# Kernel tuning notes

Measured on AMD Instinct MI355X. Metric: run time of the kernel, lower is better.

The kernel has to match this reference:

```python
import jax, jax.numpy as jnp
import numpy as np

N_NODES = 100000
N_EDGES = 6400000


def setup_inputs() -> dict:
    key = jax.random.key(0)
    ks = jax.random.split(key, 8)
    x = jax.random.normal(ks[0], (N_NODES, 1), dtype=jnp.float32)
    edge_index = jax.random.randint(ks[1], (2, N_EDGES), 0, N_NODES, dtype=jnp.int64)
    # lin1: Linear(1, 16); lin2: Linear(16, 1); sage lin_l: Linear(1, 2, bias=False)
    W1 = jax.random.normal(ks[2], (16, 1), dtype=jnp.float32) * 0.5
    b1 = jax.random.normal(ks[3], (16,), dtype=jnp.float32) * 0.1
    W2 = jax.random.normal(ks[4], (1, 16), dtype=jnp.float32) * 0.25
    b2 = jax.random.normal(ks[5], (1,), dtype=jnp.float32) * 0.1
    Ws = jax.random.normal(ks[6], (2, 1), dtype=jnp.float32) * 0.5
    return {"x": x, "W1": W1, "b1": b1, "W2": W2, "b2": b2, "Ws": Ws,
            "edge_index": edge_index}


def reference(x, W1, b1, W2, b2, Ws, edge_index):
    # tiny MLP: Linear(1,16) -> ReLU -> Linear(16,1)
    h = jax.nn.relu(x @ W1.T + b1) @ W2.T + b2              # [N, 1]
    src, dst = edge_index[0], edge_index[1]
    # SAGEConv mean aggregation: mean of source features per target node
    msg = h[src]                                            # [E, 1] gather
    agg = jax.ops.segment_sum(msg, dst, num_segments=N_NODES)   # [N, 1]
    cnt = jax.ops.segment_sum(jnp.ones((src.shape[0],), jnp.float32), dst,
                              num_segments=N_NODES)         # [N]
    mean = agg / jnp.maximum(cnt, 1.0)[:, None]             # zero for isolated nodes
    # lin_l (root_weight=False, bias=False)
    return mean @ Ws.T                                      # [N, 2]
```

## Files before the change

kernel.cpp:

```cpp
#include <hip/hip_runtime.h>

#define N_NODES 100000
#define N_EDGES 6400000

#define HSCALE 4096.0f
#define HCLAMP 63.0f
#define HBIAS  (1 << 19)

#define QBIN       4096
#define QBIN_SHIFT 12
#define NQBINS     25
#define PBLOCKS    512
#define PTHREADS   1024
#define LCAP       640
#define GBINCAP    270336
#define NQBLK      20
#define QTHREADS   1024

__global__ void mlp_kernel(const float* __restrict__ x,
                           const float* __restrict__ W1,
                           const float* __restrict__ b1,
                           const float* __restrict__ W2,
                           const float* __restrict__ b2,
                           int* __restrict__ hfix, int n) {
    int i = blockIdx.x * blockDim.x + threadIdx.x;
    if (i >= n) return;
    float xv = x[i];
    float acc = b2[0];
#pragma unroll
    for (int k = 0; k < 16; ++k) {
        float t = fmaxf(W1[k] * xv + b1[k], 0.0f);
        acc = fmaf(W2[k], t, acc);
    }
    acc = fminf(fmaxf(acc, -HCLAMP), HCLAMP);
    hfix[i] = __float2int_rn(acc * HSCALE);
}

__global__ __launch_bounds__(PTHREADS)
void partition_kernel(const int* __restrict__ src,
                      const int* __restrict__ dst,
                      const int* __restrict__ hfix,
                      unsigned* __restrict__ recs,
                      unsigned* __restrict__ cursor) {
    extern __shared__ unsigned sbuf[];
    __shared__ unsigned scnt[NQBINS];
    __shared__ unsigned sbase[NQBINS];
    const int tid = threadIdx.x;
    if (tid < NQBINS) scnt[tid] = 0u;
    __syncthreads();

    const int quads = (N_EDGES / 4) / PBLOCKS;
    const int4* __restrict__ s4 = (const int4*)src + (size_t)blockIdx.x * quads;
    const int4* __restrict__ d4 = (const int4*)dst + (size_t)blockIdx.x * quads;

    for (int i = tid; i < quads; i += PTHREADS) {
        int4 d = d4[i];
        int4 s = s4[i];
        unsigned v0 = (unsigned)(hfix[s.x] + HBIAS);
        unsigned v1 = (unsigned)(hfix[s.y] + HBIAS);
        unsigned v2 = (unsigned)(hfix[s.z] + HBIAS);
        unsigned v3 = (unsigned)(hfix[s.w] + HBIAS);
        int b0 = d.x >> QBIN_SHIFT, b1 = d.y >> QBIN_SHIFT;
        int b2 = d.z >> QBIN_SHIFT, b3 = d.w >> QBIN_SHIFT;
        unsigned rec0 = ((unsigned)(d.x & (QBIN - 1)) << 20) | v0;
        unsigned rec1 = ((unsigned)(d.y & (QBIN - 1)) << 20) | v1;
        unsigned rec2 = ((unsigned)(d.z & (QBIN - 1)) << 20) | v2;
        unsigned rec3 = ((unsigned)(d.w & (QBIN - 1)) << 20) | v3;
        unsigned sl0 = atomicAdd(&scnt[b0], 1u);
        unsigned sl1 = atomicAdd(&scnt[b1], 1u);
        unsigned sl2 = atomicAdd(&scnt[b2], 1u);
        unsigned sl3 = atomicAdd(&scnt[b3], 1u);
#define STORE(B, SL, REC)                                                     \
        if ((SL) < (unsigned)LCAP) {                                          \
            sbuf[(B) * LCAP + (SL)] = (REC);                                  \
        } else {                                                              \
            unsigned g = atomicAdd(&cursor[B], 1u);                           \
            if (g < (unsigned)GBINCAP) recs[(size_t)(B) * GBINCAP + g] = (REC);\
        }
        STORE(b0, sl0, rec0);
        STORE(b1, sl1, rec1);
        STORE(b2, sl2, rec2);
        STORE(b3, sl3, rec3);
#undef STORE
    }
    __syncthreads();

    if (tid < NQBINS) {
        unsigned m = min(scnt[tid], (unsigned)LCAP);
        sbase[tid] = atomicAdd(&cursor[tid], m);
    }
    __syncthreads();
    for (int b = 0; b < NQBINS; ++b) {
        unsigned m = min(scnt[b], (unsigned)LCAP);
        unsigned bs = sbase[b];
        for (unsigned t = tid; t < m; t += PTHREADS) {
            unsigned g = bs + t;
            if (g < (unsigned)GBINCAP)
                recs[(size_t)b * GBINCAP + g] = sbuf[b * LCAP + t];
        }
    }
}

__global__ __launch_bounds__(QTHREADS)
void accumulate_kernel(const unsigned* __restrict__ recs,
                       const unsigned* __restrict__ cursor,
                       unsigned* __restrict__ partials) {
    __shared__ unsigned acc[QBIN];
    const int b = blockIdx.x / NQBLK;
    const int j = blockIdx.x % NQBLK;
    const int tid = threadIdx.x;
    for (int k = tid; k < QBIN; k += QTHREADS) acc[k] = 0u;
    __syncthreads();

    const unsigned total = min(cursor[b], (unsigned)GBINCAP);
    const unsigned* __restrict__ base = recs + (size_t)b * GBINCAP;
    for (unsigned i = (unsigned)j * QTHREADS + tid; i < total;
         i += (unsigned)NQBLK * QTHREADS) {
        unsigned rec = base[i];
        unsigned rel = rec >> 20;
        int hf = (int)(rec & 0xFFFFFu) - HBIAS;
        atomicAdd(&acc[rel], (((unsigned)hf) << 8) + 1u);
    }
    __syncthreads();

    unsigned* __restrict__ outp = partials + (size_t)blockIdx.x * QBIN;
    for (int k = tid; k < QBIN; k += QTHREADS) outp[k] = acc[k];
}

__global__ void finalize_part(const unsigned* __restrict__ partials,
                              const float* __restrict__ Ws,
                              float* __restrict__ out, int n) {
    int i = blockIdx.x * blockDim.x + threadIdx.x;
    if (i >= n) return;
    const int bin = i >> QBIN_SHIFT;
    const int local = i & (QBIN - 1);
    int cnt = 0, sum = 0;
#pragma unroll
    for (int j = 0; j < NQBLK; ++j) {
        unsigned p = partials[(size_t)(bin * NQBLK + j) * QBIN + local];
        cnt += (int)(p & 0xFFu);
        sum += ((int)p) >> 8;
    }
    float mean = ((float)sum * (1.0f / HSCALE)) / (float)max(cnt, 1);
    float2 o;
    o.x = mean * Ws[0];
    o.y = mean * Ws[1];
    ((float2*)out)[i] = o;
}

template <int TBIN, int TNBINS>
__global__ __launch_bounds__(1024)
void scatter_binned(const int* __restrict__ src,
                    const int* __restrict__ dst,
                    const int* __restrict__ hfix,
                    unsigned* __restrict__ partials,
                    int n4_per_slice) {
    extern __shared__ unsigned acc[];
    const int bin   = blockIdx.x % TNBINS;
    const int slice = blockIdx.x / TNBINS;
    const int tid = threadIdx.x;
    for (int j = tid; j < TBIN; j += 1024) acc[j] = 0u;
    __syncthreads();
    const int bin_lo = bin * TBIN;
    const int4* __restrict__ s4 = (const int4*)src + (size_t)slice * n4_per_slice;
    const int4* __restrict__ d4 = (const int4*)dst + (size_t)slice * n4_per_slice;
#define PROC(dd, ss)                                                          \
    {                                                                         \
        unsigned r;                                                           \
        r = (unsigned)((dd).x - bin_lo);                                      \
        if (r < (unsigned)TBIN)                                               \
            atomicAdd(&acc[r], (((unsigned)hfix[(ss).x]) << 8) + 1u);         \
        r = (unsigned)((dd).y - bin_lo);                                      \
        if (r < (unsigned)TBIN)                                               \
            atomicAdd(&acc[r], (((unsigned)hfix[(ss).y]) << 8) + 1u);         \
        r = (unsigned)((dd).z - bin_lo);                                      \
        if (r < (unsigned)TBIN)                                               \
            atomicAdd(&acc[r], (((unsigned)hfix[(ss).z]) << 8) + 1u);         \
        r = (unsigned)((dd).w - bin_lo);                                      \
        if (r < (unsigned)TBIN)                                               \
            atomicAdd(&acc[r], (((unsigned)hfix[(ss).w]) << 8) + 1u);         \
    }
    for (int i = tid; i < n4_per_slice; i += 2048) {
        int4 d0 = d4[i];
        int4 s0 = s4[i];
        const int i1 = i + 1024;
        int4 d1, s1;
        const bool have1 = i1 < n4_per_slice;
        if (have1) { d1 = d4[i1]; s1 = s4[i1]; }
        PROC(d0, s0);
        if (have1) PROC(d1, s1);
    }
#undef PROC
    __syncthreads();
    unsigned* __restrict__ outp = partials + (size_t)blockIdx.x * TBIN;
    for (int j = tid; j < TBIN; j += 1024) outp[j] = acc[j];
}

template <int TBIN, int TNBINS>
__global__ void finalize_binned(const unsigned* __restrict__ partials,
                                const float* __restrict__ Ws,
                                float* __restrict__ out, int n, int nslices) {
    int i = blockIdx.x * blockDim.x + threadIdx.x;
    if (i >= n) return;
    const int bin = i / TBIN;
    const int local = i % TBIN;
    int cnt = 0, sum = 0;
    for (int s = 0; s < nslices; ++s) {
        unsigned p = partials[(size_t)(s * TNBINS + bin) * TBIN + local];
        cnt += (int)(p & 0xFFu);
        sum += ((int)p) >> 8;
    }
    float mean = ((float)sum * (1.0f / HSCALE)) / (float)max(cnt, 1);
    float2 o;
    o.x = mean * Ws[0];
    o.y = mean * Ws[1];
    ((float2*)out)[i] = o;
}

__global__ void scatter_atomic(const int* __restrict__ src,
                               const int* __restrict__ dst,
                               const int* __restrict__ hfix,
                               unsigned long long* __restrict__ packed) {
    int tid = blockIdx.x * blockDim.x + threadIdx.x;
    int stride = gridDim.x * blockDim.x;
    const int4* __restrict__ src4 = (const int4*)src;
    const int4* __restrict__ dst4 = (const int4*)dst;
    const int n4 = N_EDGES / 4;
    for (int e = tid; e < n4; e += stride) {
        int4 s = src4[e];
        int4 d = dst4[e];
        long long h0 = hfix[s.x], h1 = hfix[s.y], h2 = hfix[s.z], h3 = hfix[s.w];
        atomicAdd(&packed[d.x], ((unsigned long long)(h0 << 20)) + 1ull);
        atomicAdd(&packed[d.y], ((unsigned long long)(h1 << 20)) + 1ull);
        atomicAdd(&packed[d.z], ((unsigned long long)(h2 << 20)) + 1ull);
        atomicAdd(&packed[d.w], ((unsigned long long)(h3 << 20)) + 1ull);
    }
}

__global__ void finalize_atomic(const unsigned long long* __restrict__ packed,
                                const float* __restrict__ Ws,
                                float* __restrict__ out, int n) {
    int i = blockIdx.x * blockDim.x + threadIdx.x;
    if (i >= n) return;
    long long p = (long long)packed[i];
    int cnt = (int)(p & 0xFFFFFll);
    long long sf = p >> 20;
    float mean = ((float)sf * (1.0f / HSCALE)) / (float)max(cnt, 1);
    float2 o;
    o.x = mean * Ws[0];
    o.y = mean * Ws[1];
    ((float2*)out)[i] = o;
}

extern "C" void kernel_launch(void* const* d_in, const int* in_sizes, int n_in,
                              void* d_out, int out_size, void* d_ws, size_t ws_size,
                              hipStream_t stream) {
    const float* x  = (const float*)d_in[0];
    const float* W1 = (const float*)d_in[1];
    const float* b1 = (const float*)d_in[2];
    const float* W2 = (const float*)d_in[3];
    const float* b2 = (const float*)d_in[4];
    const float* Ws = (const float*)d_in[5];
    const int*   ei = (const int*)d_in[6];
    const int* src = ei;
    const int* dst = ei + N_EDGES;
    float* out = (float*)d_out;

    const int blk = 256;
    const int nblk_nodes = (N_NODES + blk - 1) / blk;

    int* hfix = (int*)d_ws;
    const size_t base = 512 * 1024;

    mlp_kernel<<<nblk_nodes, blk, 0, stream>>>(x, W1, b1, W2, b2, hfix, N_NODES);

    const size_t curs_off = base;
    const size_t recs_off = base + 4096;
    const size_t recs_bytes = (size_t)NQBINS * GBINCAP * sizeof(unsigned);
    const size_t part_off = recs_off + recs_bytes;
    const size_t part_bytes = (size_t)NQBINS * NQBLK * QBIN * sizeof(unsigned);
    const size_t need_part = part_off + part_bytes;

    if (ws_size >= need_part) {
        unsigned* cursor   = (unsigned*)((char*)d_ws + curs_off);
        unsigned* recs     = (unsigned*)((char*)d_ws + recs_off);
        unsigned* partials = (unsigned*)((char*)d_ws + part_off);

        (void)hipFuncSetAttribute(
            reinterpret_cast<const void*>(&partition_kernel),
            hipFuncAttributeMaxDynamicSharedMemorySize,
            NQBINS * LCAP * (int)sizeof(unsigned));

        hipMemsetAsync((void*)cursor, 0, NQBINS * sizeof(unsigned), stream);
        partition_kernel<<<PBLOCKS, PTHREADS,
                           NQBINS * LCAP * sizeof(unsigned), stream>>>(
            src, dst, hfix, recs, cursor);
        accumulate_kernel<<<NQBINS * NQBLK, QTHREADS, 0, stream>>>(
            recs, cursor, partials);
        finalize_part<<<nblk_nodes, blk, 0, stream>>>(partials, Ws, out, N_NODES);
        return;
    }

    constexpr int BIN3 = 33792;
    constexpr int NB3 = 3;
    (void)hipFuncSetAttribute(
        reinterpret_cast<const void*>(&scatter_binned<BIN3, NB3>),
        hipFuncAttributeMaxDynamicSharedMemorySize, BIN3 * sizeof(unsigned));
    unsigned* partials = (unsigned*)((char*)d_ws + base);
    const int cands3[3] = {80, 64, 32};
    for (int c = 0; c < 3; ++c) {
        int G3 = cands3[c];
        if (ws_size < base + (size_t)G3 * NB3 * BIN3 * sizeof(unsigned)) continue;
        int n4s = (N_EDGES / 4) / G3;
        scatter_binned<BIN3, NB3>
            <<<G3 * NB3, 1024, BIN3 * sizeof(unsigned), stream>>>(
                src, dst, hfix, partials, n4s);
        finalize_binned<BIN3, NB3><<<nblk_nodes, blk, 0, stream>>>(
            partials, Ws, out, N_NODES, G3);
        return;
    }

    unsigned long long* packed = (unsigned long long*)((char*)d_ws + base);
    hipMemsetAsync((void*)packed, 0, (size_t)N_NODES * sizeof(unsigned long long),
                   stream);
    scatter_atomic<<<2048, blk, 0, stream>>>(src, dst, hfix, packed);
    finalize_atomic<<<nblk_nodes, blk, 0, stream>>>(packed, Ws, out, N_NODES);
}
```

Before: 59.56 us.

## Move hfix gather from partition pass to accumulate pass, pack src index in records

```diff
diff --git a/kernel.cpp b/kernel.cpp
--- a/kernel.cpp
+++ b/kernel.cpp
@@ -5,17 +5,18 @@
 
 #define HSCALE 4096.0f
 #define HCLAMP 63.0f
-#define HBIAS  (1 << 19)
 
 #define QBIN       4096
 #define QBIN_SHIFT 12
 #define NQBINS     25
-#define PBLOCKS    512
+#define PBLOCKS    256
 #define PTHREADS   1024
-#define LCAP       640
+#define LCAP       1280
 #define GBINCAP    270336
 #define NQBLK      20
 #define QTHREADS   1024
+
+typedef int int4v __attribute__((ext_vector_type(4)));
 
 __global__ void mlp_kernel(const float* __restrict__ x,
                            const float* __restrict__ W1,
@@ -39,7 +40,6 @@
 __global__ __launch_bounds__(PTHREADS)
 void partition_kernel(const int* __restrict__ src,
                       const int* __restrict__ dst,
-                      const int* __restrict__ hfix,
                       unsigned* __restrict__ recs,
                       unsigned* __restrict__ cursor) {
     extern __shared__ unsigned sbuf[];
@@ -50,22 +50,18 @@
     __syncthreads();
 
     const int quads = (N_EDGES / 4) / PBLOCKS;
-    const int4* __restrict__ s4 = (const int4*)src + (size_t)blockIdx.x * quads;
-    const int4* __restrict__ d4 = (const int4*)dst + (size_t)blockIdx.x * quads;
+    const int4v* __restrict__ s4 = (const int4v*)src + (size_t)blockIdx.x * quads;
+    const int4v* __restrict__ d4 = (const int4v*)dst + (size_t)blockIdx.x * quads;
 
     for (int i = tid; i < quads; i += PTHREADS) {
-        int4 d = d4[i];
-        int4 s = s4[i];
-        unsigned v0 = (unsigned)(hfix[s.x] + HBIAS);
-        unsigned v1 = (unsigned)(hfix[s.y] + HBIAS);
-        unsigned v2 = (unsigned)(hfix[s.z] + HBIAS);
-        unsigned v3 = (unsigned)(hfix[s.w] + HBIAS);
+        int4v d = __builtin_nontemporal_load(d4 + i);
+        int4v s = __builtin_nontemporal_load(s4 + i);
         int b0 = d.x >> QBIN_SHIFT, b1 = d.y >> QBIN_SHIFT;
         int b2 = d.z >> QBIN_SHIFT, b3 = d.w >> QBIN_SHIFT;
-        unsigned rec0 = ((unsigned)(d.x & (QBIN - 1)) << 20) | v0;
-        unsigned rec1 = ((unsigned)(d.y & (QBIN - 1)) << 20) | v1;
-        unsigned rec2 = ((unsigned)(d.z & (QBIN - 1)) << 20) | v2;
-        unsigned rec3 = ((unsigned)(d.w & (QBIN - 1)) << 20) | v3;
+        unsigned rec0 = ((unsigned)s.x << 12) | (unsigned)(d.x & (QBIN - 1));
+        unsigned rec1 = ((unsigned)s.y << 12) | (unsigned)(d.y & (QBIN - 1));
+        unsigned rec2 = ((unsigned)s.z << 12) | (unsigned)(d.z & (QBIN - 1));
+        unsigned rec3 = ((unsigned)s.w << 12) | (unsigned)(d.w & (QBIN - 1));
         unsigned sl0 = atomicAdd(&scnt[b0], 1u);
         unsigned sl1 = atomicAdd(&scnt[b1], 1u);
         unsigned sl2 = atomicAdd(&scnt[b2], 1u);
@@ -104,6 +100,7 @@
 __global__ __launch_bounds__(QTHREADS)
 void accumulate_kernel(const unsigned* __restrict__ recs,
                        const unsigned* __restrict__ cursor,
+                       const int* __restrict__ hfix,
                        unsigned* __restrict__ partials) {
     __shared__ unsigned acc[QBIN];
     const int b = blockIdx.x / NQBLK;
@@ -117,8 +114,9 @@
     for (unsigned i = (unsigned)j * QTHREADS + tid; i < total;
          i += (unsigned)NQBLK * QTHREADS) {
         unsigned rec = base[i];
-        unsigned rel = rec >> 20;
-        int hf = (int)(rec & 0xFFFFFu) - HBIAS;
+        unsigned srcn = rec >> 12;
+        unsigned rel = rec & (QBIN - 1);
+        int hf = hfix[srcn];
         atomicAdd(&acc[rel], (((unsigned)hf) << 8) + 1u);
     }
     __syncthreads();
@@ -294,9 +292,9 @@
         hipMemsetAsync((void*)cursor, 0, NQBINS * sizeof(unsigned), stream);
         partition_kernel<<<PBLOCKS, PTHREADS,
                            NQBINS * LCAP * sizeof(unsigned), stream>>>(
-            src, dst, hfix, recs, cursor);
+            src, dst, recs, cursor);
         accumulate_kernel<<<NQBINS * NQBLK, QTHREADS, 0, stream>>>(
-            recs, cursor, partials);
+            recs, cursor, hfix, partials);
         finalize_part<<<nblk_nodes, blk, 0, stream>>>(partials, Ws, out, N_NODES);
         return;
     }
```

Result: slower. 66.83 us (+12.2%).
